# Optimization experiments

Hardware: AMD Instinct MI355X
Metric: run time of the kernel (lower is better)

## Reference

```python
import jax, jax.numpy as jnp
import numpy as np

N_HEADS = 4
D_K = 64
SCALE = D_K ** (-0.5)


def setup_inputs() -> dict:
    key = jax.random.key(0)
    k1, k2, k3, k4, k5 = jax.random.split(key, 5)
    B, C, H, W = 16, 256, 32, 32
    x = jax.random.normal(k1, (B, C, H, W), dtype=jnp.float32)
    # Linear weights stored as (in, out) for x @ W convention
    w_qkv = jax.random.normal(k2, (C, N_HEADS * D_K * 3), dtype=jnp.float32) * (C ** -0.5)
    b_qkv = jax.random.normal(k3, (N_HEADS * D_K * 3,), dtype=jnp.float32) * 0.02
    w_out = jax.random.normal(k4, (N_HEADS * D_K, C), dtype=jnp.float32) * ((N_HEADS * D_K) ** -0.5)
    b_out = jax.random.normal(k5, (C,), dtype=jnp.float32) * 0.02
    return {"x": x, "w_qkv": w_qkv, "b_qkv": b_qkv, "w_out": w_out, "b_out": b_out}


def reference(x, w_qkv, b_qkv, w_out, b_out):
    # NOTE: the original torch module defines GroupNorm but never applies it
    # in forward; we faithfully reproduce the forward as written.
    B, C, H, W = x.shape
    S = H * W
    xs = x.reshape(B, C, S).transpose(0, 2, 1)            # [B, S, C]
    qkv = (xs @ w_qkv + b_qkv).reshape(B, S, N_HEADS, 3 * D_K)
    q, k, v = jnp.split(qkv, 3, axis=-1)                   # each [B, S, H, d_k]
    attn = jnp.einsum('bihd,bjhd->bijh', q, k) * SCALE     # [B, S, S, H]
    attn = jax.nn.softmax(attn, axis=2)                    # softmax over j (keys)
    res = jnp.einsum('bijh,bjhd->bihd', attn, v)           # [B, S, H, d_k]
    res = res.reshape(B, S, N_HEADS * D_K)
    res = res @ w_out + b_out + xs                         # residual add
    return res.transpose(0, 2, 1).reshape(B, C, H, W)
```

## Files before the change

kernel.cpp:

```cpp
#include <hip/hip_runtime.h>
#include <hip/hip_bf16.h>

typedef __attribute__((ext_vector_type(8))) short short8;
typedef __attribute__((ext_vector_type(4))) float floatx4;
typedef unsigned short u16;

#define SCL_LOG2E 0.1803368801111204f

__device__ inline u16 f2b(float f) {
  __hip_bfloat16 h = __float2bfloat16(f);
  union { __hip_bfloat16 h; u16 u; } cv; cv.h = h; return cv.u;
}
__device__ inline float b2f(u16 u) {
  union { u16 u; __hip_bfloat16 h; } cv; cv.u = u; return __bfloat162float(cv.h);
}

__global__ __launch_bounds__(256) void tr_f32_bf16(const float* __restrict__ in,
                                                   u16* __restrict__ out, int R, int Cc) {
  __shared__ u16 tile[32][33];
  int bz = blockIdx.z;
  const float* inb = in + (size_t)bz * R * Cc;
  u16* outb = out + (size_t)bz * R * Cc;
  int c0 = blockIdx.x * 32, r0 = blockIdx.y * 32;
  int tx = threadIdx.x, ty = threadIdx.y;
#pragma unroll
  for (int i = 0; i < 32; i += 8)
    tile[ty + i][tx] = f2b(inb[(size_t)(r0 + ty + i) * Cc + c0 + tx]);
  __syncthreads();
#pragma unroll
  for (int i = 0; i < 32; i += 8)
    outb[(size_t)(c0 + ty + i) * R + r0 + tx] = tile[tx][ty + i];
}

__global__ __launch_bounds__(256) void tr64_f32_bf16(const float* __restrict__ in,
                                                     u16* __restrict__ out,
                                                     int R, int Cc) {
  __shared__ u16 tile[64][72];
  int bz = blockIdx.z;
  const float* inb = in + (size_t)bz * R * Cc;
  u16* outb = out + (size_t)bz * R * Cc;
  int c0 = blockIdx.x * 64, r0 = blockIdx.y * 64;
  int tx = threadIdx.x, ty = threadIdx.y;
#pragma unroll
  for (int i = 0; i < 4; i++) {
    int r = ty + 16 * i;
    float4 v = *(const float4*)&inb[(size_t)(r0 + r) * Cc + c0 + tx * 4];
    tile[tx * 4 + 0][r] = f2b(v.x);
    tile[tx * 4 + 1][r] = f2b(v.y);
    tile[tx * 4 + 2][r] = f2b(v.z);
    tile[tx * 4 + 3][r] = f2b(v.w);
  }
  __syncthreads();
#pragma unroll
  for (int i = 0; i < 4; i++) {
    int cc = ty + 16 * i;
    ushort4 o = *(ushort4*)&tile[cc][tx * 4];
    *(ushort4*)&outb[(size_t)(c0 + cc) * R + r0 + tx * 4] = o;
  }
}

__global__ __launch_bounds__(256) void qkv_gemm(const u16* __restrict__ xs,
                                                const u16* __restrict__ wT,
                                                const float* __restrict__ bias,
                                                u16* __restrict__ Qo,
                                                u16* __restrict__ Ko,
                                                u16* __restrict__ Vto) {
  __shared__ u16 As[128 * 32];
  __shared__ u16 Bs[128 * 32];
  const int tid = threadIdx.x, wave = tid >> 6, lane = tid & 63;
  const int l15 = lane & 15, quad = lane >> 4;
  const int wm = (wave >> 1) * 64, wn = (wave & 1) * 64;
  const int m0 = blockIdx.x * 128, n0 = blockIdx.y * 128;

  floatx4 acc[4][4] = {};
  const int srow = wave * 32 + (lane >> 2);
  const int scol = (lane & 3) * 8;

  for (int kt = 0; kt < 256; kt += 32) {
#pragma unroll
    for (int i = 0; i < 2; i++) {
      int r = srow + i * 16;
      *(short8*)&As[r * 32 + scol] =
          *(const short8*)&xs[(size_t)(m0 + r) * 256 + kt + scol];
      *(short8*)&Bs[r * 32 + scol] =
          *(const short8*)&wT[(size_t)(n0 + r) * 256 + kt + scol];
    }
    __syncthreads();
    short8 af[4], bfr[4];
#pragma unroll
    for (int mi = 0; mi < 4; mi++)
      af[mi] = *(short8*)&As[(wm + mi * 16 + l15) * 32 + quad * 8];
#pragma unroll
    for (int ni = 0; ni < 4; ni++)
      bfr[ni] = *(short8*)&Bs[(wn + ni * 16 + l15) * 32 + quad * 8];
#pragma unroll
    for (int mi = 0; mi < 4; mi++)
#pragma unroll
      for (int ni = 0; ni < 4; ni++)
        acc[mi][ni] = __builtin_amdgcn_mfma_f32_16x16x32_bf16(af[mi], bfr[ni],
                                                              acc[mi][ni], 0, 0, 0);
    __syncthreads();
  }

#pragma unroll
  for (int ni = 0; ni < 4; ni++) {
    int n = n0 + wn + ni * 16 + l15;
    float bv = bias[n];
    int h = n / 192;
    int rem = n - h * 192;
#pragma unroll
    for (int mi = 0; mi < 4; mi++) {
      int gm = m0 + wm + mi * 16 + quad * 4;
      int bb = gm >> 10, s = gm & 1023;
      if (rem < 128) {
        u16* dst;
        float scl;
        if (rem < 64) { dst = Qo; scl = SCL_LOG2E; } else { dst = Ko; scl = 1.0f; }
        int d = rem & 63;
#pragma unroll
        for (int r = 0; r < 4; r++)
          dst[((size_t)(bb * 4 + h) * 1024 + s + r) * 64 + d] =
              f2b((acc[mi][ni][r] + bv) * scl);
      } else {
        int d = rem - 128;
        ushort4 pk;
        pk.x = f2b(acc[mi][ni][0] + bv);
        pk.y = f2b(acc[mi][ni][1] + bv);
        pk.z = f2b(acc[mi][ni][2] + bv);
        pk.w = f2b(acc[mi][ni][3] + bv);
        *(ushort4*)&Vto[((size_t)(bb * 4 + h) * 64 + d) * 1024 + s] = pk;
      }
    }
  }
}

__global__ __launch_bounds__(256) void attn_kern(const u16* __restrict__ Q,
                                                 const u16* __restrict__ K,
                                                 const u16* __restrict__ Vt,
                                                 u16* __restrict__ O) {
  __shared__ u16 Ks[64 * 72];
  __shared__ u16 Vs[64 * 72];
  __shared__ u16 Ps[4 * 32 * 72];
  const int bh = blockIdx.y;
  const u16* Qp = Q + (size_t)bh * 64 * 1024;
  const u16* Kp = K + (size_t)bh * 64 * 1024;
  const u16* Vp = Vt + (size_t)bh * 64 * 1024;
  u16* Op = O + (size_t)bh * 64 * 1024;
  const int q0 = blockIdx.x * 128;
  const int tid = threadIdx.x, wave = tid >> 6, lane = tid & 63;
  const int l15 = lane & 15, quad = lane >> 4;
  const int wrow = q0 + wave * 32;

  short8 qa[2][2];
#pragma unroll
  for (int mi = 0; mi < 2; mi++)
#pragma unroll
    for (int ks = 0; ks < 2; ks++)
      qa[mi][ks] =
          *(const short8*)&Qp[(size_t)(wrow + mi * 16 + l15) * 64 + ks * 32 + quad * 8];

  float lrow[2][4] = {};
  floatx4 acc[2][4] = {};

  const int srow = wave * 16 + (lane >> 3);
  const int scol = (lane & 7) * 8;

  for (int j0 = 0; j0 < 1024; j0 += 64) {
#pragma unroll
    for (int i = 0; i < 2; i++) {
      int r = srow + i * 8;
      *(short8*)&Ks[r * 72 + scol] = *(const short8*)&Kp[(size_t)(j0 + r) * 64 + scol];
      *(short8*)&Vs[r * 72 + scol] = *(const short8*)&Vp[(size_t)r * 1024 + j0 + scol];
    }
    __syncthreads();

    floatx4 sf[2][4] = {};
    short8 kb[4][2];
#pragma unroll
    for (int nj = 0; nj < 4; nj++)
#pragma unroll
      for (int ks = 0; ks < 2; ks++)
        kb[nj][ks] = *(short8*)&Ks[(nj * 16 + l15) * 72 + ks * 32 + quad * 8];
#pragma unroll
    for (int mi = 0; mi < 2; mi++)
#pragma unroll
      for (int nj = 0; nj < 4; nj++)
#pragma unroll
        for (int ks = 0; ks < 2; ks++)
          sf[mi][nj] = __builtin_amdgcn_mfma_f32_16x16x32_bf16(qa[mi][ks], kb[nj][ks],
                                                               sf[mi][nj], 0, 0, 0);

#pragma unroll
    for (int mi = 0; mi < 2; mi++)
#pragma unroll
      for (int nj = 0; nj < 4; nj++)
#pragma unroll
        for (int r = 0; r < 4; r++) {
          float p = exp2f(sf[mi][nj][r]);
          lrow[mi][r] += p;
          Ps[wave * 32 * 72 + (mi * 16 + quad * 4 + r) * 72 + nj * 16 + l15] = f2b(p);
        }

    short8 pa[2][2], vb[4][2];
#pragma unroll
    for (int mi = 0; mi < 2; mi++)
#pragma unroll
      for (int ks = 0; ks < 2; ks++)
        pa[mi][ks] =
            *(short8*)&Ps[wave * 32 * 72 + (mi * 16 + l15) * 72 + ks * 32 + quad * 8];
#pragma unroll
    for (int db = 0; db < 4; db++)
#pragma unroll
      for (int ks = 0; ks < 2; ks++)
        vb[db][ks] = *(short8*)&Vs[(db * 16 + l15) * 72 + ks * 32 + quad * 8];
#pragma unroll
    for (int mi = 0; mi < 2; mi++)
#pragma unroll
      for (int db = 0; db < 4; db++)
#pragma unroll
        for (int ks = 0; ks < 2; ks++)
          acc[mi][db] = __builtin_amdgcn_mfma_f32_16x16x32_bf16(pa[mi][ks], vb[db][ks],
                                                                acc[mi][db], 0, 0, 0);
    __syncthreads();
  }

#pragma unroll
  for (int mi = 0; mi < 2; mi++)
#pragma unroll
    for (int d = 1; d < 16; d <<= 1)
#pragma unroll
      for (int r = 0; r < 4; r++)
        lrow[mi][r] += __shfl_xor(lrow[mi][r], d, 64);

#pragma unroll
  for (int mi = 0; mi < 2; mi++) {
    float inv[4];
#pragma unroll
    for (int r = 0; r < 4; r++) inv[r] = 1.f / lrow[mi][r];
#pragma unroll
    for (int db = 0; db < 4; db++)
#pragma unroll
      for (int r = 0; r < 4; r++)
        Op[(size_t)(wrow + mi * 16 + quad * 4 + r) * 64 + db * 16 + l15] =
            f2b(acc[mi][db][r] * inv[r]);
  }
}

__global__ __launch_bounds__(256) void out_gemm(const u16* __restrict__ Oin,
                                                const u16* __restrict__ wT,
                                                const float* __restrict__ bias,
                                                const float* __restrict__ x,
                                                float* __restrict__ out) {
  __shared__ u16 As[128 * 32];
  __shared__ u16 Bs[128 * 32];
  const int tid = threadIdx.x, wave = tid >> 6, lane = tid & 63;
  const int l15 = lane & 15, quad = lane >> 4;
  const int wm = (wave >> 1) * 64, wn = (wave & 1) * 64;
  const int m0 = blockIdx.x * 128, n0 = blockIdx.y * 128;
  const int bb = m0 >> 10;

  floatx4 acc[4][4] = {};
  const int srow = wave * 32 + (lane >> 2);
  const int scol = (lane & 3) * 8;

  for (int kt = 0; kt < 256; kt += 32) {
    int h = kt >> 6, d0 = kt & 63;
#pragma unroll
    for (int i = 0; i < 2; i++) {
      int r = srow + i * 16;
      int s = (m0 + r) & 1023;
      *(short8*)&As[r * 32 + scol] =
          *(const short8*)&Oin[((size_t)(bb * 4 + h) * 1024 + s) * 64 + d0 + scol];
      *(short8*)&Bs[r * 32 + scol] =
          *(const short8*)&wT[(size_t)(n0 + r) * 256 + kt + scol];
    }
    __syncthreads();
    short8 af[4], bfr[4];
#pragma unroll
    for (int mi = 0; mi < 4; mi++)
      af[mi] = *(short8*)&As[(wm + mi * 16 + l15) * 32 + quad * 8];
#pragma unroll
    for (int ni = 0; ni < 4; ni++)
      bfr[ni] = *(short8*)&Bs[(wn + ni * 16 + l15) * 32 + quad * 8];
#pragma unroll
    for (int mi = 0; mi < 4; mi++)
#pragma unroll
      for (int ni = 0; ni < 4; ni++)
        acc[mi][ni] = __builtin_amdgcn_mfma_f32_16x16x32_bf16(af[mi], bfr[ni],
                                                              acc[mi][ni], 0, 0, 0);
    __syncthreads();
  }

#pragma unroll
  for (int ni = 0; ni < 4; ni++) {
    int c = n0 + wn + ni * 16 + l15;
    float bv = bias[c];
#pragma unroll
    for (int mi = 0; mi < 4; mi++) {
      int gm = m0 + wm + mi * 16 + quad * 4;
      int s = gm & 1023;
      size_t idx = ((size_t)bb * 256 + c) * 1024 + s;
      float4 xr = *(const float4*)&x[idx];
      float4 o;
      o.x = acc[mi][ni][0] + bv + xr.x;
      o.y = acc[mi][ni][1] + bv + xr.y;
      o.z = acc[mi][ni][2] + bv + xr.z;
      o.w = acc[mi][ni][3] + bv + xr.w;
      *(float4*)&out[idx] = o;
    }
  }
}

extern "C" void kernel_launch(void* const* d_in, const int* in_sizes, int n_in,
                              void* d_out, int out_size, void* d_ws, size_t ws_size,
                              hipStream_t stream) {
  const float* x     = (const float*)d_in[0];
  const float* w_qkv = (const float*)d_in[1];
  const float* b_qkv = (const float*)d_in[2];
  const float* w_out = (const float*)d_in[3];
  const float* b_out = (const float*)d_in[4];
  float* out = (float*)d_out;
  char* ws = (char*)d_ws;

  u16* xs    = (u16*)(ws);
  u16* wqkvT = (u16*)(ws + 8388608);
  u16* woutT = (u16*)(ws + 8388608 + 393216);
  u16* Qb    = (u16*)(ws + 8912896);
  u16* Kb    = (u16*)(ws + 8912896 + 8388608);
  u16* Vtb   = (u16*)(ws + 8912896 + 16777216);
  u16* Ob    = xs;

  tr64_f32_bf16<<<dim3(16, 4, 16), dim3(16, 16), 0, stream>>>(x, xs, 256, 1024);
  tr_f32_bf16<<<dim3(24, 8, 1), dim3(32, 8), 0, stream>>>(w_qkv, wqkvT, 256, 768);
  tr_f32_bf16<<<dim3(8, 8, 1), dim3(32, 8), 0, stream>>>(w_out, woutT, 256, 256);
  qkv_gemm<<<dim3(128, 6), 256, 0, stream>>>(xs, wqkvT, b_qkv, Qb, Kb, Vtb);
  attn_kern<<<dim3(8, 64), 256, 0, stream>>>(Qb, Kb, Vtb, Ob);
  out_gemm<<<dim3(128, 2), 256, 0, stream>>>(Ob, woutT, b_out, x, out);
}
```

Baseline: 158.7 us.

## Restructure attention kernel with transposed S, register P, and double-buffered K/V

The attention kernel now computes the transposed score tile (K·Qᵀ), so the exp'd probabilities land in registers already laid out as the B operand of a 16x16x16 MFMA. This removes the per-wave P round trip through shared memory. K/V tiles are double-buffered, with the next tile prefetched into registers during compute, which cuts one barrier per iteration. Each block now handles 64 queries instead of 128, doubling the grid, and output is staged through LDS for coalesced stores. The cost is more total K/V loads across blocks and smaller MFMAs for the PV product.

Result: faster. 145.0 us (-8.7%).

```diff
diff --git a/kernel.cpp b/kernel.cpp
--- a/kernel.cpp
+++ b/kernel.cpp
@@ -2,6 +2,7 @@
 #include <hip/hip_bf16.h>
 
 typedef __attribute__((ext_vector_type(8))) short short8;
+typedef __attribute__((ext_vector_type(4))) short short4v;
 typedef __attribute__((ext_vector_type(4))) float floatx4;
 typedef unsigned short u16;
 
@@ -134,115 +135,116 @@
   }
 }
 
-__global__ __launch_bounds__(256) void attn_kern(const u16* __restrict__ Q,
-                                                 const u16* __restrict__ K,
-                                                 const u16* __restrict__ Vt,
-                                                 u16* __restrict__ O) {
-  __shared__ u16 Ks[64 * 72];
-  __shared__ u16 Vs[64 * 72];
-  __shared__ u16 Ps[4 * 32 * 72];
+__global__ __launch_bounds__(256, 4) void attn_kern(const u16* __restrict__ Q,
+                                                    const u16* __restrict__ K,
+                                                    const u16* __restrict__ Vt,
+                                                    u16* __restrict__ O) {
+  __shared__ u16 kv[2 * 2 * 64 * 72];
   const int bh = blockIdx.y;
   const u16* Qp = Q + (size_t)bh * 64 * 1024;
   const u16* Kp = K + (size_t)bh * 64 * 1024;
   const u16* Vp = Vt + (size_t)bh * 64 * 1024;
   u16* Op = O + (size_t)bh * 64 * 1024;
-  const int q0 = blockIdx.x * 128;
+  const int q0 = blockIdx.x * 64;
   const int tid = threadIdx.x, wave = tid >> 6, lane = tid & 63;
   const int l15 = lane & 15, quad = lane >> 4;
-  const int wrow = q0 + wave * 32;
-
-  short8 qa[2][2];
-#pragma unroll
-  for (int mi = 0; mi < 2; mi++)
-#pragma unroll
-    for (int ks = 0; ks < 2; ks++)
-      qa[mi][ks] =
-          *(const short8*)&Qp[(size_t)(wrow + mi * 16 + l15) * 64 + ks * 32 + quad * 8];
-
-  float lrow[2][4] = {};
-  floatx4 acc[2][4] = {};
-
-  const int srow = wave * 16 + (lane >> 3);
-  const int scol = (lane & 7) * 8;
-
-  for (int j0 = 0; j0 < 1024; j0 += 64) {
-#pragma unroll
-    for (int i = 0; i < 2; i++) {
-      int r = srow + i * 8;
-      *(short8*)&Ks[r * 72 + scol] = *(const short8*)&Kp[(size_t)(j0 + r) * 64 + scol];
-      *(short8*)&Vs[r * 72 + scol] = *(const short8*)&Vp[(size_t)r * 1024 + j0 + scol];
-    }
-    __syncthreads();
-
-    floatx4 sf[2][4] = {};
-    short8 kb[4][2];
-#pragma unroll
-    for (int nj = 0; nj < 4; nj++)
-#pragma unroll
-      for (int ks = 0; ks < 2; ks++)
-        kb[nj][ks] = *(short8*)&Ks[(nj * 16 + l15) * 72 + ks * 32 + quad * 8];
-#pragma unroll
-    for (int mi = 0; mi < 2; mi++)
-#pragma unroll
-      for (int nj = 0; nj < 4; nj++)
-#pragma unroll
-        for (int ks = 0; ks < 2; ks++)
-          sf[mi][nj] = __builtin_amdgcn_mfma_f32_16x16x32_bf16(qa[mi][ks], kb[nj][ks],
-                                                               sf[mi][nj], 0, 0, 0);
-
-#pragma unroll
-    for (int mi = 0; mi < 2; mi++)
-#pragma unroll
-      for (int nj = 0; nj < 4; nj++)
-#pragma unroll
-        for (int r = 0; r < 4; r++) {
-          float p = exp2f(sf[mi][nj][r]);
-          lrow[mi][r] += p;
-          Ps[wave * 32 * 72 + (mi * 16 + quad * 4 + r) * 72 + nj * 16 + l15] = f2b(p);
-        }
-
-    short8 pa[2][2], vb[4][2];
-#pragma unroll
-    for (int mi = 0; mi < 2; mi++)
-#pragma unroll
-      for (int ks = 0; ks < 2; ks++)
-        pa[mi][ks] =
-            *(short8*)&Ps[wave * 32 * 72 + (mi * 16 + l15) * 72 + ks * 32 + quad * 8];
-#pragma unroll
-    for (int db = 0; db < 4; db++)
-#pragma unroll
-      for (int ks = 0; ks < 2; ks++)
-        vb[db][ks] = *(short8*)&Vs[(db * 16 + l15) * 72 + ks * 32 + quad * 8];
-#pragma unroll
-    for (int mi = 0; mi < 2; mi++)
-#pragma unroll
-      for (int db = 0; db < 4; db++)
-#pragma unroll
-        for (int ks = 0; ks < 2; ks++)
-          acc[mi][db] = __builtin_amdgcn_mfma_f32_16x16x32_bf16(pa[mi][ks], vb[db][ks],
-                                                                acc[mi][db], 0, 0, 0);
-    __syncthreads();
-  }
-
-#pragma unroll
-  for (int mi = 0; mi < 2; mi++)
-#pragma unroll
-    for (int d = 1; d < 16; d <<= 1)
-#pragma unroll
-      for (int r = 0; r < 4; r++)
-        lrow[mi][r] += __shfl_xor(lrow[mi][r], d, 64);
-
-#pragma unroll
-  for (int mi = 0; mi < 2; mi++) {
-    float inv[4];
-#pragma unroll
-    for (int r = 0; r < 4; r++) inv[r] = 1.f / lrow[mi][r];
-#pragma unroll
-    for (int db = 0; db < 4; db++)
-#pragma unroll
-      for (int r = 0; r < 4; r++)
-        Op[(size_t)(wrow + mi * 16 + quad * 4 + r) * 64 + db * 16 + l15] =
-            f2b(acc[mi][db][r] * inv[r]);
+
+  short8 qa[2];
+#pragma unroll
+  for (int ks = 0; ks < 2; ks++)
+    qa[ks] = *(const short8*)&Qp[(size_t)(q0 + wave * 16 + l15) * 64 + ks * 32 + quad * 8];
+
+  const int srow = tid >> 2;
+  const int sc = (tid & 3) * 16;
+
+  {
+    short8 k0 = *(const short8*)&Kp[(size_t)srow * 64 + sc];
+    short8 k1 = *(const short8*)&Kp[(size_t)srow * 64 + sc + 8];
+    short8 v0 = *(const short8*)&Vp[(size_t)srow * 1024 + sc];
+    short8 v1 = *(const short8*)&Vp[(size_t)srow * 1024 + sc + 8];
+    *(short8*)&kv[srow * 72 + sc] = k0;
+    *(short8*)&kv[srow * 72 + sc + 8] = k1;
+    *(short8*)&kv[4608 + srow * 72 + sc] = v0;
+    *(short8*)&kv[4608 + srow * 72 + sc + 8] = v1;
+  }
+  __syncthreads();
+
+  float lsum = 0.f;
+  floatx4 acc[4] = {};
+
+  for (int t = 0; t < 16; t++) {
+    const u16* Ksb = kv + (t & 1) * 9216;
+    const u16* Vsb = Ksb + 4608;
+
+    short8 nk0, nk1, nv0, nv1;
+    if (t < 15) {
+      nk0 = *(const short8*)&Kp[(size_t)((t + 1) * 64 + srow) * 64 + sc];
+      nk1 = *(const short8*)&Kp[(size_t)((t + 1) * 64 + srow) * 64 + sc + 8];
+      nv0 = *(const short8*)&Vp[(size_t)srow * 1024 + (t + 1) * 64 + sc];
+      nv1 = *(const short8*)&Vp[(size_t)srow * 1024 + (t + 1) * 64 + sc + 8];
+    }
+
+    floatx4 sf[4];
+#pragma unroll
+    for (int mj = 0; mj < 4; mj++) {
+      short8 kb0 = *(const short8*)&Ksb[(mj * 16 + l15) * 72 + quad * 8];
+      short8 kb1 = *(const short8*)&Ksb[(mj * 16 + l15) * 72 + 32 + quad * 8];
+      floatx4 z = {};
+      z = __builtin_amdgcn_mfma_f32_16x16x32_bf16(kb0, qa[0], z, 0, 0, 0);
+      sf[mj] = __builtin_amdgcn_mfma_f32_16x16x32_bf16(kb1, qa[1], z, 0, 0, 0);
+    }
+
+    short4v pb[4];
+#pragma unroll
+    for (int mj = 0; mj < 4; mj++) {
+      float p0 = exp2f(sf[mj][0]), p1 = exp2f(sf[mj][1]);
+      float p2 = exp2f(sf[mj][2]), p3 = exp2f(sf[mj][3]);
+      lsum += (p0 + p1) + (p2 + p3);
+      short4v pk;
+      pk[0] = (short)f2b(p0); pk[1] = (short)f2b(p1);
+      pk[2] = (short)f2b(p2); pk[3] = (short)f2b(p3);
+      pb[mj] = pk;
+    }
+
+#pragma unroll
+    for (int c = 0; c < 4; c++)
+#pragma unroll
+      for (int md = 0; md < 4; md++) {
+        short4v va = *(const short4v*)&Vsb[(md * 16 + l15) * 72 + c * 16 + quad * 4];
+        acc[md] = __builtin_amdgcn_mfma_f32_16x16x16bf16_1k(va, pb[c], acc[md], 0, 0, 0);
+      }
+
+    if (t < 15) {
+      u16* dst = kv + ((t + 1) & 1) * 9216;
+      *(short8*)&dst[srow * 72 + sc] = nk0;
+      *(short8*)&dst[srow * 72 + sc + 8] = nk1;
+      *(short8*)&dst[4608 + srow * 72 + sc] = nv0;
+      *(short8*)&dst[4608 + srow * 72 + sc + 8] = nv1;
+    }
+    __syncthreads();
+  }
+
+  lsum += __shfl_xor(lsum, 16, 64);
+  lsum += __shfl_xor(lsum, 32, 64);
+  float inv = 1.f / lsum;
+
+  __syncthreads();
+  u16* Ot = kv;
+#pragma unroll
+  for (int md = 0; md < 4; md++) {
+    uint2 pk;
+    u16 a0 = f2b(acc[md][0] * inv), a1 = f2b(acc[md][1] * inv);
+    u16 a2 = f2b(acc[md][2] * inv), a3 = f2b(acc[md][3] * inv);
+    pk.x = (unsigned)a0 | ((unsigned)a1 << 16);
+    pk.y = (unsigned)a2 | ((unsigned)a3 << 16);
+    *(uint2*)&Ot[(wave * 16 + l15) * 72 + md * 16 + quad * 4] = pk;
+  }
+#pragma unroll
+  for (int h = 0; h < 2; h++) {
+    int row = h * 8 + (lane >> 3);
+    int col = (lane & 7) * 8;
+    short8 v = *(const short8*)&Ot[(wave * 16 + row) * 72 + col];
+    *(short8*)&Op[(size_t)(q0 + wave * 16 + row) * 64 + col] = v;
   }
 }
 
@@ -334,6 +336,6 @@
   tr_f32_bf16<<<dim3(24, 8, 1), dim3(32, 8), 0, stream>>>(w_qkv, wqkvT, 256, 768);
   tr_f32_bf16<<<dim3(8, 8, 1), dim3(32, 8), 0, stream>>>(w_out, woutT, 256, 256);
   qkv_gemm<<<dim3(128, 6), 256, 0, stream>>>(xs, wqkvT, b_qkv, Qb, Kb, Vtb);
-  attn_kern<<<dim3(8, 64), 256, 0, stream>>>(Qb, Kb, Vtb, Ob);
+  attn_kern<<<dim3(16, 64), 256, 0, stream>>>(Qb, Kb, Vtb, Ob);
   out_gemm<<<dim3(128, 2), 256, 0, stream>>>(Ob, woutT, b_out, x, out);
 }
```
